# Kernel tuning notes

Hardware: AMD Instinct MI355X
Metric: run time of the kernel (lower is better)

Reference implementation:

```python
import jax, jax.numpy as jnp
import numpy as np

STATE = 13  # fixed PBM state size from pbm_temp_from_sensor
HID = 64    # DDM hidden width


def setup_inputs() -> dict:
    key = jax.random.key(0)
    ks = jax.random.split(key, 11)
    B, P = 65536, 32
    T_room = 20.0 + jax.random.normal(ks[0], (B, STATE), jnp.float32)
    T_wall = 18.0 + jax.random.normal(ks[1], (B, STATE), jnp.float32)
    T_out = 5.0 + jax.random.normal(ks[2], (B, P), jnp.float32)
    door = jax.random.uniform(ks[3], (B, P), dtype=jnp.float32)
    timing = jax.random.uniform(ks[4], (B, P), dtype=jnp.float32)
    # PBM coupling coefficients (learned, per state node)
    k_rw = jax.random.uniform(ks[5], (STATE,), dtype=jnp.float32) * 0.1
    k_ro = jax.random.uniform(ks[6], (STATE,), dtype=jnp.float32) * 0.05
    k_wr = jax.random.uniform(ks[7], (STATE,), dtype=jnp.float32) * 0.1
    k_wo = jax.random.uniform(ks[8], (STATE,), dtype=jnp.float32) * 0.05
    # DDM: MLP on concat(T_room_hat, T_wall_hat, T_out_i, door_i, timing_i) -> 29 feats
    IN = 2 * STATE + 3
    W1 = jax.random.normal(ks[9], (IN, HID), jnp.float32) / np.sqrt(IN)
    b1 = jnp.zeros((HID,), jnp.float32)
    W2 = jax.random.normal(ks[10], (HID, STATE), jnp.float32) / np.sqrt(HID)
    b2 = jnp.zeros((STATE,), jnp.float32)
    return dict(T_room=T_room, T_wall=T_wall, T_out=T_out, door=door, timing=timing,
                k_rw=k_rw, k_ro=k_ro, k_wr=k_wr, k_wo=k_wo,
                W1=W1, b1=b1, W2=W2, b2=b2,
                N=15, delta_t=60, num_preds=32)


def reference(T_room, T_wall, T_out, door, timing,
              k_rw, k_ro, k_wr, k_wo, W1, b1, W2, b2,
              N, delta_t, num_preds):
    # NOTE on faithfulness: the torch forward re-clones T_room_new/T_wall_new from the
    # ORIGINAL T_room/T_wall at the top of every outer iteration i, so only the last
    # iteration (i = num_preds-1) survives in the returned tensors; all earlier rows
    # equal the untouched inputs. We reproduce exactly that output.
    s = delta_t / 3600.0  # RC time-constant scaling

    def pbm(Tr, Tw, To, src):
        Tr_n = Tr + s * ((Tw - Tr) * k_rw + (To - Tr) * k_ro + src)
        Tw_n = Tw + s * ((Tr - Tw) * k_wr + (To - Tw) * k_wo)
        return Tr_n, Tw_n

    def ddm(Tr, Tw, To, d, t):
        # [B, 29] -> [B, HID] -> [B, 13]
        x = jnp.concatenate([Tr, Tw, jnp.broadcast_to(To, Tr.shape[:1] + (1,)),
                             d[:, None], t[:, None]], axis=-1)
        h = jax.nn.relu(x @ W1 + b1)
        return (h @ W2 + b2) * 0.01

    i = num_preds - 1
    To = T_out[:, i][:, None]      # [B, 1], broadcasts over the 13 state dims
    d_i = door[:, i]               # [B]
    t_i = timing[:, i]             # [B]

    def step(carry, _):
        Tr, Tw = carry
        Tr_hat, Tw_hat = pbm(Tr, Tw, To, 0.0)          # uncorrected PBM step
        src = ddm(Tr_hat, Tw_hat, To, d_i, t_i)        # corrective source term
        return pbm(Tr, Tw, To, src), None              # corrected PBM step

    (Tr_f, Tw_f), _ = jax.lax.scan(step, (T_room, T_wall), None, length=N)

    P = num_preds
    T_room_new = jnp.tile(T_room[None], (P, 1, 1)).at[P - 1].set(Tr_f)  # [P, B, 13]
    T_wall_new = jnp.tile(T_wall[None], (P, 1, 1)).at[P - 1].set(Tw_f)
    return T_room_new, T_wall_new
```

## Files before the change

kernel.cpp:

```cpp
#include <hip/hip_runtime.h>


#define STATE 13
#define HID   64
#define PRED  32
#define NSTEP 15

typedef float    f32x4 __attribute__((ext_vector_type(4)));
typedef short    s16x8 __attribute__((ext_vector_type(8)));
typedef unsigned u32x2 __attribute__((ext_vector_type(2)));
typedef float    vfloat4 __attribute__((ext_vector_type(4)));

constexpr int B      = 65536;
constexpr int B13    = B * STATE;
constexpr int B13_4  = B13 / 4;
constexpr int CBLK   = B / 64;

constexpr int WS_W1F = 0;
constexpr int WS_W2F = 4096;
constexpr int WS_B1C = 6144;
constexpr int WS_B2C = 10240;
constexpr int WS_SK  = 11264;

__device__ __forceinline__ unsigned short f2bf(float f) {
    return __builtin_bit_cast(unsigned short, (__bf16)f);
}
__device__ __forceinline__ unsigned pkbf(float lo, float hi) {
    return (unsigned)f2bf(lo) | ((unsigned)f2bf(hi) << 16);
}
__device__ __forceinline__ float bflo(unsigned u) { return __builtin_bit_cast(float, u << 16); }
__device__ __forceinline__ float bfhi(unsigned u) { return __builtin_bit_cast(float, u & 0xffff0000u); }

__global__ __launch_bounds__(256) void ffcosta_prep(
    const float* __restrict__ W1, const float* __restrict__ b1,
    const float* __restrict__ W2, const float* __restrict__ b2,
    const float* __restrict__ k_rw, const float* __restrict__ k_ro,
    const float* __restrict__ k_wr, const float* __restrict__ k_wo,
    char* __restrict__ ws)
{
    const int tid = threadIdx.x;
    const float s = 60.0f / 3600.0f;

    unsigned short* w1f = (unsigned short*)(ws + WS_W1F);
    for (int idx = tid; idx < 4*64*8; idx += 256) {
        const int t = idx >> 9, l = (idx >> 3) & 63, r = idx & 7;
        const int nd = 8*(l>>4) + r;
        const int j  = 16*t + (l & 15);
        float v = 0.0f;
        if (nd < 13)       v = W1[nd*HID + j];
        else if (nd >= 16) v = W1[(nd-3)*HID + j];
        w1f[idx] = f2bf(v);
    }
    unsigned short* w2f = (unsigned short*)(ws + WS_W2F);
    for (int idx = tid; idx < 2*64*8; idx += 256) {
        const int sl = idx >> 9, l = (idx >> 3) & 63, r = idx & 7;
        const int j = 32*sl + 8*(l>>4) + r;
        const int c = l & 15;
        w2f[idx] = (c < STATE) ? f2bf(W2[j*STATE + c]) : (unsigned short)0;
    }
    float* b1c = (float*)(ws + WS_B1C);
    for (int idx = tid; idx < 4*64*4; idx += 256) {
        const int t = idx >> 8, l = (idx >> 2) & 63, r = idx & 3;
        b1c[idx] = b1[16*t + 4*(l>>4) + r];
    }
    float* b2c = (float*)(ws + WS_B2C);
    for (int idx = tid; idx < 64*4; idx += 256) {
        const int l = idx >> 2, r = idx & 3;
        const int c = 4*(l>>4) + r;
        b2c[idx] = (c < STATE) ? b2[c] : 0.0f;
    }
    float* sk = (float*)(ws + WS_SK);
    for (int idx = tid; idx < 4*64*4; idx += 256) {
        const int a = idx >> 8, l = (idx >> 2) & 63, r = idx & 3;
        const int c = 4*(l>>4) + r;
        const float* ka = (a==0)? k_rw : (a==1)? k_ro : (a==2)? k_wr : k_wo;
        sk[idx] = (c < STATE) ? s * ka[c] : 0.0f;
    }
}

__global__ __launch_bounds__(256) void ffcosta_kernel(
    const float* __restrict__ T_room, const float* __restrict__ T_wall,
    const float* __restrict__ T_out,  const float* __restrict__ door,
    const float* __restrict__ timing,
    const char*  __restrict__ ws,
    float* __restrict__ out)
{
    __shared__ __align__(16) char smem[4 * 6144];

    const int tid  = threadIdx.x;
    const int lane = tid & 63, w = tid >> 6;
    const int el   = lane & 15, hi = lane >> 4;
    const int e    = blockIdx.x * 64 + w * 16 + el;

    s16x8 w1a[4], w2a[2];
    f32x4 b1c[4], b2c, skrw, skro, skwr, skwo;
    #pragma unroll
    for (int t = 0; t < 4; ++t) {
        w1a[t] = *(const s16x8*)(ws + WS_W1F + (t*64 + lane)*16);
        b1c[t] = *(const f32x4*)(ws + WS_B1C + (t*64 + lane)*16);
    }
    #pragma unroll
    for (int sl = 0; sl < 2; ++sl)
        w2a[sl] = *(const s16x8*)(ws + WS_W2F + (sl*64 + lane)*16);
    b2c  = *(const f32x4*)(ws + WS_B2C + lane*16);
    skrw = *(const f32x4*)(ws + WS_SK +        lane*16);
    skro = *(const f32x4*)(ws + WS_SK + 1024 + lane*16);
    skwr = *(const f32x4*)(ws + WS_SK + 2048 + lane*16);
    skwo = *(const f32x4*)(ws + WS_SK + 3072 + lane*16);

    const int off4 = (hi < 3) ? 4*hi : 9;
    f32x4 vr, vw;
    __builtin_memcpy(&vr, T_room + e*STATE + off4, 16);
    __builtin_memcpy(&vw, T_wall + e*STATE + off4, 16);
    const float To = T_out [e*PRED + (PRED-1)];
    const float dv = door  [e*PRED + (PRED-1)];
    const float tv = timing[e*PRED + (PRED-1)];
    float Tr[4], Tw[4];
    if (hi < 3) {
        Tr[0]=vr[0]; Tr[1]=vr[1]; Tr[2]=vr[2]; Tr[3]=vr[3];
        Tw[0]=vw[0]; Tw[1]=vw[1]; Tw[2]=vw[2]; Tw[3]=vw[3];
    } else {
        Tr[0]=vr[3]; Tr[1]=0.0f; Tr[2]=0.0f; Tr[3]=0.0f;
        Tw[0]=vw[3]; Tw[1]=To;   Tw[2]=dv;   Tw[3]=tv;
    }

    const int  cf = blockIdx.x * 256 + tid;
    const bool cvalid = cf < B13_4;
    vfloat4 crm = {0,0,0,0}, cwl = {0,0,0,0};
    if (cvalid) {
        crm = ((const vfloat4*)T_room)[cf];
        cwl = ((const vfloat4*)T_wall)[cf];
    }
    vfloat4* out0_4 = (vfloat4*)out;
    vfloat4* out1_4 = (vfloat4*)(out + (size_t)PRED * B13);

    const int wb = w * 6144;
    const int xk = (el & 3) << 4;
    const int hk = (el & 7) << 4;
    const int a_xw_tr = wb + el*64 + (( 8*hi) ^ xk);
    const int a_xw_tw = wb + el*64 + ((32 + 8*hi) ^ xk);
    const int a_xr    = wb + el*64 + ((16*hi) ^ xk);
    int a_hw[4], a_hr[2];
    #pragma unroll
    for (int t = 0; t < 4; ++t) a_hw[t] = wb + 2048 + el*128 + ((32*t + 8*hi) ^ hk);
    #pragma unroll
    for (int sl = 0; sl < 2; ++sl) a_hr[sl] = wb + 2048 + el*128 + ((64*sl + 16*hi) ^ hk);

    const float s001 = (60.0f/3600.0f) * 0.01f;

    #pragma unroll 1
    for (int n = 0; n < NSTEP; ++n) {
        if (cvalid) {
            const int i0 = (2*n) * B13_4 + cf;
            __builtin_nontemporal_store(crm, out0_4 + i0);
            __builtin_nontemporal_store(crm, out0_4 + i0 + B13_4);
            __builtin_nontemporal_store(cwl, out1_4 + i0);
            __builtin_nontemporal_store(cwl, out1_4 + i0 + B13_4);
        }

        #pragma unroll
        for (int r = 0; r < 4; ++r) {
            const float dA = Tw[r] - Tr[r];
            const float dB = To    - Tr[r];
            const float dC = To    - Tw[r];
            Tr[r] = fmaf(dB, skro[r], fmaf(dA, skrw[r], Tr[r]));
            Tw[r] = fmaf(dC, skwo[r], fmaf(-dA, skwr[r], Tw[r]));
        }

        const unsigned tr01 = pkbf(Tr[0], Tr[1]), tr23 = pkbf(Tr[2], Tr[3]);
        const unsigned tw01 = pkbf(Tw[0], Tw[1]), tw23 = pkbf(Tw[2], Tw[3]);
        u32x2 v;
        v[0]=tr01; v[1]=tr23; *(u32x2*)(smem + a_xw_tr) = v;
        v[0]=tw01; v[1]=tw23; *(u32x2*)(smem + a_xw_tw) = v;
        v[0]=pkbf(Tr[0]-bflo(tr01), Tr[1]-bfhi(tr01));
        v[1]=pkbf(Tr[2]-bflo(tr23), Tr[3]-bfhi(tr23));
        *(u32x2*)(smem + a_xw_tr + 1024) = v;
        v[0]=pkbf(Tw[0]-bflo(tw01), Tw[1]-bfhi(tw01));
        v[1]=pkbf(Tw[2]-bflo(tw23), Tw[3]-bfhi(tw23));
        *(u32x2*)(smem + a_xw_tw + 1024) = v;

        const s16x8 xbh = *(const s16x8*)(smem + a_xr);
        const s16x8 xbl = *(const s16x8*)(smem + a_xr + 1024);

        f32x4 acc[4];
        #pragma unroll
        for (int t = 0; t < 4; ++t) {
            acc[t] = __builtin_amdgcn_mfma_f32_16x16x32_bf16(w1a[t], xbh, b1c[t], 0, 0, 0);
            acc[t] = __builtin_amdgcn_mfma_f32_16x16x32_bf16(w1a[t], xbl, acc[t], 0, 0, 0);
        }

        #pragma unroll
        for (int t = 0; t < 4; ++t) {
            const float h0 = fmaxf(acc[t][0], 0.0f), h1 = fmaxf(acc[t][1], 0.0f);
            const float h2 = fmaxf(acc[t][2], 0.0f), h3 = fmaxf(acc[t][3], 0.0f);
            const unsigned p01 = pkbf(h0, h1), p23 = pkbf(h2, h3);
            u32x2 hv; hv[0]=p01; hv[1]=p23;
            *(u32x2*)(smem + a_hw[t]) = hv;
            hv[0] = pkbf(h0-bflo(p01), h1-bfhi(p01));
            hv[1] = pkbf(h2-bflo(p23), h3-bfhi(p23));
            *(u32x2*)(smem + a_hw[t] + 2048) = hv;
        }

        const s16x8 hb0 = *(const s16x8*)(smem + a_hr[0]);
        const s16x8 hb1 = *(const s16x8*)(smem + a_hr[1]);
        const s16x8 hl0 = *(const s16x8*)(smem + a_hr[0] + 2048);
        const s16x8 hl1 = *(const s16x8*)(smem + a_hr[1] + 2048);

        f32x4 sv = b2c;
        sv = __builtin_amdgcn_mfma_f32_16x16x32_bf16(w2a[0], hb0, sv, 0, 0, 0);
        sv = __builtin_amdgcn_mfma_f32_16x16x32_bf16(w2a[1], hb1, sv, 0, 0, 0);
        sv = __builtin_amdgcn_mfma_f32_16x16x32_bf16(w2a[0], hl0, sv, 0, 0, 0);
        sv = __builtin_amdgcn_mfma_f32_16x16x32_bf16(w2a[1], hl1, sv, 0, 0, 0);

        #pragma unroll
        for (int r = 0; r < 4; ++r) Tr[r] = fmaf(sv[r], s001, Tr[r]);
    }

    if (cvalid) {
        const int i0 = 30 * B13_4 + cf;
        __builtin_nontemporal_store(crm, out0_4 + i0);
        __builtin_nontemporal_store(cwl, out1_4 + i0);
    }

    float* p0 = out + (size_t)(PRED-1) * B13 + e*STATE;
    float* p1 = p0 + (size_t)PRED * B13;
    if (hi < 3) {
        f32x4 s0, s1;
        s0[0]=Tr[0]; s0[1]=Tr[1]; s0[2]=Tr[2]; s0[3]=Tr[3];
        s1[0]=Tw[0]; s1[1]=Tw[1]; s1[2]=Tw[2]; s1[3]=Tw[3];
        __builtin_memcpy(p0 + 4*hi, &s0, 16);
        __builtin_memcpy(p1 + 4*hi, &s1, 16);
    } else {
        p0[12] = Tr[0];
        p1[12] = Tw[0];
    }
}

extern "C" void kernel_launch(void* const* d_in, const int* in_sizes, int n_in,
                              void* d_out, int out_size, void* d_ws, size_t ws_size,
                              hipStream_t stream) {
    const float* T_room = (const float*)d_in[0];
    const float* T_wall = (const float*)d_in[1];
    const float* T_out  = (const float*)d_in[2];
    const float* door   = (const float*)d_in[3];
    const float* timing = (const float*)d_in[4];
    const float* k_rw   = (const float*)d_in[5];
    const float* k_ro   = (const float*)d_in[6];
    const float* k_wr   = (const float*)d_in[7];
    const float* k_wo   = (const float*)d_in[8];
    const float* W1     = (const float*)d_in[9];
    const float* b1     = (const float*)d_in[10];
    const float* W2     = (const float*)d_in[11];
    const float* b2     = (const float*)d_in[12];
    float* out = (float*)d_out;
    char*  ws  = (char*)d_ws;

    ffcosta_prep<<<1, 256, 0, stream>>>(W1, b1, W2, b2, k_rw, k_ro, k_wr, k_wo, ws);
    ffcosta_kernel<<<CBLK, 256, 0, stream>>>(
        T_room, T_wall, T_out, door, timing, ws, out);
}
```

Baseline: 287.3 us.

## Split output-copy stores into dedicated blocks separate from compute blocks

The broadcast copy of the inputs into the 31 untouched output slices was interleaved with the MLP step loop inside the compute blocks. It now runs in its own set of blocks (the first CPB block indices), each streaming its row to every slice and then returning. The compute blocks are offset in the grid and do only the scan. The intent is to let store-bound and compute-bound work run concurrently on different CUs rather than serialising the stores inside each compute wave. The trade-off is that scheduling order now decides how well the two kinds of work overlap.

```diff
diff --git a/kernel.cpp b/kernel.cpp
--- a/kernel.cpp
+++ b/kernel.cpp
@@ -14,6 +14,7 @@
 constexpr int B      = 65536;
 constexpr int B13    = B * STATE;
 constexpr int B13_4  = B13 / 4;
+constexpr int CPB    = B13_4 / 256;
 constexpr int CBLK   = B / 64;
 
 constexpr int WS_W1F = 0;
@@ -87,10 +88,29 @@
 {
     __shared__ __align__(16) char smem[4 * 6144];
 
+    float* out0 = out;
+    float* out1 = out + (size_t)PRED * B13;
+
+    if (blockIdx.x < CPB) {
+        const int ct = blockIdx.x * 256 + threadIdx.x;
+        const vfloat4 r = ((const vfloat4*)T_room)[ct];
+        const vfloat4 w = ((const vfloat4*)T_wall)[ct];
+        vfloat4* o0 = (vfloat4*)out0 + ct;
+        vfloat4* o1 = (vfloat4*)out1 + ct;
+        #pragma unroll 1
+        for (int p = 0; p < PRED - 1; ++p) {
+            __builtin_nontemporal_store(r, o0);
+            __builtin_nontemporal_store(w, o1);
+            o0 += B13_4;
+            o1 += B13_4;
+        }
+        return;
+    }
+
     const int tid  = threadIdx.x;
     const int lane = tid & 63, w = tid >> 6;
     const int el   = lane & 15, hi = lane >> 4;
-    const int e    = blockIdx.x * 64 + w * 16 + el;
+    const int e    = (blockIdx.x - CPB) * 64 + w * 16 + el;
 
     s16x8 w1a[4], w2a[2];
     f32x4 b1c[4], b2c, skrw, skro, skwr, skwo;
@@ -124,16 +144,6 @@
         Tw[0]=vw[3]; Tw[1]=To;   Tw[2]=dv;   Tw[3]=tv;
     }
 
-    const int  cf = blockIdx.x * 256 + tid;
-    const bool cvalid = cf < B13_4;
-    vfloat4 crm = {0,0,0,0}, cwl = {0,0,0,0};
-    if (cvalid) {
-        crm = ((const vfloat4*)T_room)[cf];
-        cwl = ((const vfloat4*)T_wall)[cf];
-    }
-    vfloat4* out0_4 = (vfloat4*)out;
-    vfloat4* out1_4 = (vfloat4*)(out + (size_t)PRED * B13);
-
     const int wb = w * 6144;
     const int xk = (el & 3) << 4;
     const int hk = (el & 7) << 4;
@@ -150,14 +160,6 @@
 
     #pragma unroll 1
     for (int n = 0; n < NSTEP; ++n) {
-        if (cvalid) {
-            const int i0 = (2*n) * B13_4 + cf;
-            __builtin_nontemporal_store(crm, out0_4 + i0);
-            __builtin_nontemporal_store(crm, out0_4 + i0 + B13_4);
-            __builtin_nontemporal_store(cwl, out1_4 + i0);
-            __builtin_nontemporal_store(cwl, out1_4 + i0 + B13_4);
-        }
-
         #pragma unroll
         for (int r = 0; r < 4; ++r) {
             const float dA = Tw[r] - Tr[r];
@@ -216,13 +218,7 @@
         for (int r = 0; r < 4; ++r) Tr[r] = fmaf(sv[r], s001, Tr[r]);
     }
 
-    if (cvalid) {
-        const int i0 = 30 * B13_4 + cf;
-        __builtin_nontemporal_store(crm, out0_4 + i0);
-        __builtin_nontemporal_store(cwl, out1_4 + i0);
-    }
-
-    float* p0 = out + (size_t)(PRED-1) * B13 + e*STATE;
+    float* p0 = out0 + (size_t)(PRED-1) * B13 + e*STATE;
     float* p1 = p0 + (size_t)PRED * B13;
     if (hi < 3) {
         f32x4 s0, s1;
@@ -256,6 +252,6 @@
     char*  ws  = (char*)d_ws;
 
     ffcosta_prep<<<1, 256, 0, stream>>>(W1, b1, W2, b2, k_rw, k_ro, k_wr, k_wo, ws);
-    ffcosta_kernel<<<CBLK, 256, 0, stream>>>(
+    ffcosta_kernel<<<CPB + CBLK, 256, 0, stream>>>(
         T_room, T_wall, T_out, door, timing, ws, out);
 }
```

New measurement: 301.0 us. 4.7% more time.
